# Kernel optimization log

Hardware: AMD Instinct MI355X
Metric: run time of the kernel (lower is better)

## Reference

```python
import jax, jax.numpy as jnp
import numpy as np

S, E, K, D = 50000, 20000, 128, 128  # students, exercises, knowledge, emb dim
NE = 800000                          # edges per polarity
B = 8192                             # batch of response logs
L = 3                                # gcn layers
TEMP, CONTROL = 0.2, 0.3


def setup_inputs() -> dict:
    key = jax.random.key(0)
    ks = jax.random.split(key, 40)

    def nrm(i, shape, scale=0.05):
        return jax.random.normal(ks[i], shape, jnp.float32) * scale

    def uni(i, shape):
        return jax.random.uniform(ks[i], shape, jnp.float32)

    inp = {
        'stu_id': jax.random.randint(ks[0], (B,), 0, S, jnp.int32),
        'exer_id': jax.random.randint(ks[1], (B,), 0, E, jnp.int32),
        'kn_emb': uni(2, (B, K)),
        'ui1_u': jax.random.randint(ks[3], (NE,), 0, S, jnp.int32),
        'ui1_i': jax.random.randint(ks[4], (NE,), 0, E, jnp.int32),
        'ui1_val': uni(5, (NE,)), 'iu1_val': uni(6, (NE,)),
        'eps_ui1': uni(7, (NE,)), 'eps_iu1': uni(8, (NE,)),
        'ui0_u': jax.random.randint(ks[9], (NE,), 0, S, jnp.int32),
        'ui0_i': jax.random.randint(ks[10], (NE,), 0, E, jnp.int32),
        'ui0_val': uni(11, (NE,)), 'iu0_val': uni(12, (NE,)),
        'eps_ui0': uni(13, (NE,)), 'eps_iu0': uni(14, (NE,)),
        # embeddings
        'student_emb': nrm(15, (S, D)), 'exercise_emb': nrm(16, (E, D)),
        'knowledge_emb': nrm(17, (K, D)),
        'stu_b': nrm(18, (S, 1)), 'exer_b': nrm(19, (E, 1)), 'disc': nrm(20, (E, 1)),
        # edge-gate MLPs (polarity 1 and 0)
        'W1_l1': nrm(21, (D, 2 * D)), 'b1_l1': jnp.zeros((D,), jnp.float32),
        'W2_l1': nrm(22, (1, D)), 'b2_l1': jnp.zeros((1,), jnp.float32),
        'W1_l0': nrm(23, (D, 2 * D)), 'b1_l0': jnp.zeros((D,), jnp.float32),
        'W2_l0': nrm(24, (1, D)), 'b2_l0': jnp.zeros((1,), jnp.float32),
        # PosLinear prednet
        'pw1': nrm(25, (256, K)), 'pb1': jnp.zeros((256,), jnp.float32),
        'pw2': nrm(26, (128, 256)), 'pb2': jnp.zeros((128,), jnp.float32),
        'pw3': nrm(27, (1, 128)), 'pb3': jnp.zeros((1,), jnp.float32),
    }
    return inp


def _gate(uids, iids, uemb, iemb, W1, b1, W2, b2, eps):
    # concrete-distribution edge gate; embeddings are detached in original code
    row = jax.lax.stop_gradient(uemb)[uids]          # [NE, D]
    col = jax.lax.stop_gradient(iemb)[iids]          # [NE, D]
    h = jax.nn.relu(jnp.concatenate([row, col], axis=1) @ W1.T + b1)
    logit = (h @ W2.T + b2).reshape(-1)              # [NE]
    eps = jnp.clip(eps, 1e-6, 1.0 - 1e-6)
    g = jnp.log(eps) - jnp.log1p(-eps)               # logistic noise
    return CONTROL * jax.nn.sigmoid((logit + g) / TEMP) + (1.0 - CONTROL)


def _spmm(rows, cols, vals, x, n_rows):
    # out[rows] += vals * x[cols]
    return jax.ops.segment_sum(vals[:, None] * x[cols], rows, num_segments=n_rows)


def _poslin(x, W, b):
    Wp = 2.0 * jax.nn.relu(-W) + W  # == |W|
    return x @ Wp.T + b


def reference(stu_id, exer_id, kn_emb, ui1_u, ui1_i, ui1_val, iu1_val, eps_ui1,
              eps_iu1, ui0_u, ui0_i, ui0_val, iu0_val, eps_ui0, eps_iu0,
              student_emb, exercise_emb, knowledge_emb, stu_b, exer_b, disc,
              W1_l1, b1_l1, W2_l1, b2_l1, W1_l0, b1_l0, W2_l0, b2_l0,
              pw1, pb1, pw2, pb2, pw3, pb3):
    # --- graph_learner: per-edge gates on all 4 sparse matrices ---
    v_ui1 = ui1_val * _gate(ui1_u, ui1_i, student_emb, exercise_emb, W1_l1, b1_l1, W2_l1, b2_l1, eps_ui1)
    v_iu1 = iu1_val * _gate(ui1_u, ui1_i, student_emb, exercise_emb, W1_l1, b1_l1, W2_l1, b2_l1, eps_iu1)
    v_ui0 = ui0_val * _gate(ui0_u, ui0_i, student_emb, exercise_emb, W1_l0, b1_l0, W2_l0, b2_l0, eps_ui0)
    v_iu0 = iu0_val * _gate(ui0_u, ui0_i, student_emb, exercise_emb, W1_l0, b1_l0, W2_l0, b2_l0, eps_iu0)

    # --- graph_representations: L rounds of sparse propagation, mean over layers ---
    stu, exer = student_emb, exercise_emb
    stu_sum, exer_sum = stu, exer
    for _ in range(L):
        u1 = _spmm(ui1_u, ui1_i, v_ui1, exer, S)
        i1 = _spmm(ui1_i, ui1_u, v_iu1, stu, E)
        u0 = _spmm(ui0_u, ui0_i, v_ui0, exer, S)
        i0 = _spmm(ui0_i, ui0_u, v_iu0, stu, E)
        stu, exer = u1 + u0, i1 + i0
        stu_sum = stu_sum + stu
        exer_sum = exer_sum + exer
    stu_final = stu_sum / (L + 1)
    exer_final = exer_sum / (L + 1)

    # --- NCDM-style prediction head with PosLinear MLP ---
    stat = jax.nn.sigmoid(stu_final[stu_id] @ knowledge_emb.T + stu_b[stu_id])   # [B, K]
    diff = jax.nn.sigmoid(exer_final[exer_id] @ knowledge_emb.T + exer_b[exer_id])
    e_d = jax.nn.sigmoid(disc[exer_id])                                          # [B, 1]
    x = e_d * (stat - diff) * kn_emb
    h = jax.nn.sigmoid(_poslin(x, pw1, pb1))
    h = jax.nn.sigmoid(_poslin(h, pw2, pb2))
    out = jax.nn.sigmoid(_poslin(h, pw3, pb3)).reshape(-1)                       # [B]
    return out
```

## Files before the change

### kernel.cpp

```cpp
#include <hip/hip_runtime.h>
#include <hip/hip_bf16.h>
#include <math.h>

#define S_N 50000
#define E_N 20000
#define K_N 128
#define D_N 128
#define NE_N 800000
#define B_N 8192
#define L_N 3
#define GATE_TILES (NE_N / 64)
#define NB_S 782
#define NB_E 313
#define BPAD 464
#define BSLACK 480

typedef __attribute__((ext_vector_type(4))) float floatx4;
typedef __attribute__((ext_vector_type(8))) short short8v;

__device__ __forceinline__ unsigned short f2bf(float x) {
  unsigned int u = __float_as_uint(x);
  u += 0x7FFFu + ((u >> 16) & 1u);
  return (unsigned short)(u >> 16);
}
__device__ __forceinline__ float bf2f(unsigned short u) {
  return __uint_as_float(((unsigned int)u) << 16);
}
__device__ __forceinline__ float sigm(float z) { return 1.0f / (1.0f + __expf(-z)); }

__device__ __forceinline__ unsigned char f2e4m3(float x) {
  unsigned int u = __float_as_uint(x);
  unsigned char s = (unsigned char)((u >> 24) & 0x80);
  int e = (int)((u >> 23) & 0xFF) - 127;
  unsigned int m = u & 0x7FFFFF;
  if (((u >> 23) & 0xFF) == 0) return s;
  if (e >= 9) return s | 0x7E;
  if (e < -10) return s;
  if (e >= -6) {
    unsigned int keep = m >> 20;
    unsigned int rest = m & 0xFFFFF;
    if (rest > 0x80000u || (rest == 0x80000u && (keep & 1))) keep++;
    if (keep == 8) { keep = 0; e++; if (e >= 9) return s | 0x7E; }
    unsigned char b = (unsigned char)(s | ((e + 7) << 3) | keep);
    if ((b & 0x7F) == 0x7F) b = s | 0x7E;
    return b;
  }
  int shift = -6 - e;
  unsigned int full = 0x800000u | m;
  unsigned int q = full >> (20 + shift);
  unsigned int rest = full & ((1u << (20 + shift)) - 1);
  unsigned int half = 1u << (19 + shift);
  if (rest > half || (rest == half && (q & 1))) q++;
  if (q == 8) return s | 0x08;
  return (unsigned char)(s | q);
}
__device__ __forceinline__ unsigned int pk4_fp8(float4 v) {
  return (unsigned int)f2e4m3(v.x) | ((unsigned int)f2e4m3(v.y) << 8) |
         ((unsigned int)f2e4m3(v.z) << 16) | ((unsigned int)f2e4m3(v.w) << 24);
}

__global__ void prep_kernel(const float* __restrict__ W1_l1, const float* __restrict__ W1_l0,
                            const float* __restrict__ pw1, const float* __restrict__ pw2,
                            const float* __restrict__ pw3, const float* __restrict__ ke,
                            unsigned int* __restrict__ w1f8_1, unsigned int* __restrict__ w1f8_0,
                            float* __restrict__ pw1T, float* __restrict__ pw2T,
                            float* __restrict__ pw3a, float* __restrict__ keT) {
  int i = blockIdx.x * blockDim.x + threadIdx.x;
  if (i < 8192) { w1f8_1[i] = pk4_fp8(((const float4*)W1_l1)[i]); return; }
  i -= 8192;
  if (i < 8192) { w1f8_0[i] = pk4_fp8(((const float4*)W1_l0)[i]); return; }
  i -= 8192;
  if (i < 32768) { int d = i >> 8, j = i & 255; pw1T[i] = fabsf(pw1[j * 128 + d]); return; }
  i -= 32768;
  if (i < 32768) { int d = i >> 7, j = i & 127; pw2T[i] = fabsf(pw2[j * 256 + d]); return; }
  i -= 32768;
  if (i < 128) { pw3a[i] = fabsf(pw3[i]); return; }
  i -= 128;
  if (i < 16384) { int d = i >> 7, k = i & 127; keT[i] = ke[k * 128 + d]; return; }
}

__global__ void init_bf_kernel(const float* __restrict__ se, const float* __restrict__ ee,
                               unsigned short* __restrict__ sbf, unsigned short* __restrict__ ebf,
                               unsigned int* __restrict__ sf8, unsigned int* __restrict__ ef8,
                               float* __restrict__ sS, float* __restrict__ eS) {
  int i = blockIdx.x * blockDim.x + threadIdx.x;
  const int nS4 = S_N * 32, nE4 = E_N * 32;
  if (i < nS4) {
    float4 v = ((const float4*)se)[i];
    ((float4*)sS)[i] = v;
    unsigned int lo = (unsigned int)f2bf(v.x) | ((unsigned int)f2bf(v.y) << 16);
    unsigned int hi = (unsigned int)f2bf(v.z) | ((unsigned int)f2bf(v.w) << 16);
    ((uint2*)sbf)[i] = make_uint2(lo, hi);
    sf8[i] = pk4_fp8(v);
    return;
  }
  i -= nS4;
  if (i < nE4) {
    float4 v = ((const float4*)ee)[i];
    ((float4*)eS)[i] = v;
    unsigned int lo = (unsigned int)f2bf(v.x) | ((unsigned int)f2bf(v.y) << 16);
    unsigned int hi = (unsigned int)f2bf(v.z) | ((unsigned int)f2bf(v.w) << 16);
    ((uint2*)ebf)[i] = make_uint2(lo, hi);
    ef8[i] = pk4_fp8(v);
  }
}

__global__ void zero_kernel(int* __restrict__ p, int n) {
  int i = blockIdx.x * blockDim.x + threadIdx.x;
  if (i < n) p[i] = 0;
}

__global__ __launch_bounds__(256)
void histB_kernel(const int* __restrict__ u1, const int* __restrict__ i1,
                  const int* __restrict__ u0, const int* __restrict__ i0,
                  int* __restrict__ gHistS, int* __restrict__ gHistE) {
  __shared__ int hS[NB_S], hE[NB_E];
  int t = threadIdx.x;
  for (int b = t; b < NB_S; b += 256) hS[b] = 0;
  for (int b = t; b < NB_E; b += 256) hE[b] = 0;
  __syncthreads();
  int e0 = blockIdx.x * 2048;
  for (int k = 0; k < 8; ++k) {
    int e = e0 + k * 256 + t;
    if (e < NE_N) {
      atomicAdd(&hS[u1[e] >> 6], 1);
      atomicAdd(&hS[u0[e] >> 6], 1);
      atomicAdd(&hE[i1[e] >> 6], 1);
      atomicAdd(&hE[i0[e] >> 6], 1);
    }
  }
  __syncthreads();
  for (int b = t; b < NB_S; b += 256) if (hS[b]) atomicAdd(&gHistS[b], hS[b]);
  for (int b = t; b < NB_E; b += 256) if (hE[b]) atomicAdd(&gHistE[b], hE[b]);
}

__global__ __launch_bounds__(128)
void scanB_kernel(const int* __restrict__ gHistS, int* __restrict__ baseS,
                  int* __restrict__ gCurS, int* __restrict__ basePS,
                  const int* __restrict__ gHistE, int* __restrict__ baseE,
                  int* __restrict__ gCurE, int* __restrict__ basePE) {
  int w = threadIdx.x >> 6, l = threadIdx.x & 63;
  int n = w ? NB_E : NB_S;
  const int* src = w ? gHistE : gHistS;
  int* bs  = w ? baseE  : baseS;
  int* cur = w ? gCurE  : gCurS;
  int* bsP = w ? basePE : basePS;
  int carry = 0, carryP = 0;
  for (int base = 0; base < n; base += 64) {
    int i = base + l;
    int v = (i < n) ? src[i] : 0;
    int p = (i < n) ? ((v + BPAD + 15) & ~15) : 0;
    int x = v, y = p;
#pragma unroll
    for (int o = 1; o < 64; o <<= 1) {
      int xx = __shfl_up(x, o, 64);
      int yy = __shfl_up(y, o, 64);
      if (l >= o) { x += xx; y += yy; }
    }
    if (i < n) {
      int ex = carry + x - v;
      bs[i] = ex; cur[i] = ex;
      bsP[i] = carryP + y - p;
    }
    carry += __shfl(x, 63, 64);
    carryP += __shfl(y, 63, 64);
  }
  if (l == 0) { bs[n] = carry; bsP[n] = carryP; }
}

__global__ __launch_bounds__(256)
void append_kernel(const int* __restrict__ u1, const int* __restrict__ i1,
                   const int* __restrict__ u0, const int* __restrict__ i0,
                   const float* __restrict__ v_ui1, const float* __restrict__ v_iu1,
                   const float* __restrict__ v_ui0, const float* __restrict__ v_iu0,
                   int* __restrict__ gCurS, int* __restrict__ gCurE,
                   int2* __restrict__ recS, int2* __restrict__ recE) {
  __shared__ int hS[NB_S], hE[NB_E];
  int t = threadIdx.x;
  for (int b = t; b < NB_S; b += 256) hS[b] = 0;
  for (int b = t; b < NB_E; b += 256) hE[b] = 0;
  __syncthreads();
  int e0 = blockIdx.x * 2048;
  for (int k = 0; k < 8; ++k) {
    int e = e0 + k * 256 + t;
    if (e < NE_N) {
      atomicAdd(&hS[u1[e] >> 6], 1);
      atomicAdd(&hS[u0[e] >> 6], 1);
      atomicAdd(&hE[i1[e] >> 6], 1);
      atomicAdd(&hE[i0[e] >> 6], 1);
    }
  }
  __syncthreads();
  for (int b = t; b < NB_S; b += 256) { int c = hS[b]; hS[b] = c ? atomicAdd(&gCurS[b], c) : 0; }
  for (int b = t; b < NB_E; b += 256) { int c = hE[b]; hE[b] = c ? atomicAdd(&gCurE[b], c) : 0; }
  __syncthreads();
  for (int k = 0; k < 8; ++k) {
    int e = e0 + k * 256 + t;
    if (e < NE_N) {
      int a = u1[e], b = i1[e], c = u0[e], d = i0[e];
      int s;
      s = atomicAdd(&hS[a >> 6], 1); recS[s] = make_int2(((a & 63) << 16) | b, __float_as_int(v_ui1[e]));
      s = atomicAdd(&hE[b >> 6], 1); recE[s] = make_int2(((b & 63) << 16) | a, __float_as_int(v_iu1[e]));
      s = atomicAdd(&hS[c >> 6], 1); recS[s] = make_int2(((c & 63) << 16) | d, __float_as_int(v_ui0[e]));
      s = atomicAdd(&hE[d >> 6], 1); recE[s] = make_int2(((d & 63) << 16) | c, __float_as_int(v_iu0[e]));
    }
  }
}

__global__ __launch_bounds__(256)
void sortRow_kernel(const int* __restrict__ baseIn, const int* __restrict__ basePad,
                    const int2* __restrict__ rin_all, int2* __restrict__ rout_all,
                    int* __restrict__ rowPtr, int* __restrict__ rowCnt8, int nRowsTot) {
  __shared__ int cntR[64], offR[64], curR[64];
  int b = blockIdx.x, t = threadIdx.x;
  int bi = baseIn[b], cnt = baseIn[b + 1] - bi;
  int bo = basePad[b];
  int row0 = b * 64;
  const int2* rin = rin_all + bi;
  int2* rout = rout_all + bo;
  if (t < 64) cntR[t] = 0;
  __syncthreads();
  for (int j = t; j < cnt; j += 256) atomicAdd(&cntR[(rin[j].x >> 16) & 63], 1);
  __syncthreads();
  if (t < 64) {
    int p = (cntR[t] + 7) & ~7;
    int x = p;
#pragma unroll
    for (int o = 1; o < 64; o <<= 1) { int y = __shfl_up(x, o, 64); if (t >= o) x += y; }
    int ex = x - p;
    offR[t] = ex; curR[t] = ex;
    if (row0 + t < nRowsTot) {
      rowPtr[row0 + t] = bo + ex;
      rowCnt8[row0 + t] = p >> 3;
    }
  }
  __syncthreads();
  for (int j = t; j < cnt; j += 256) {
    int2 rc = rin[j];
    int r = (rc.x >> 16) & 63;
    int slot = atomicAdd(&curR[r], 1);
    rout[slot] = make_int2(rc.x & 0xFFFF, rc.y);
  }
  __syncthreads();
  if (t < 64) {
    int c = cntR[t], p = (c + 7) & ~7, o = offR[t];
    for (int j = c; j < p; ++j) rout[o + j] = make_int2(0, 0);
  }
}

__global__ __launch_bounds__(512, 2)
void gate_kernel(const int* __restrict__ eu1, const int* __restrict__ ei1,
                 const int* __restrict__ eu0, const int* __restrict__ ei0,
                 const unsigned char* __restrict__ sf8, const unsigned char* __restrict__ ef8,
                 const unsigned char* __restrict__ w1f8_1, const unsigned char* __restrict__ w1f8_0,
                 const float* __restrict__ b1_1, const float* __restrict__ w2_1,
                 const float* __restrict__ b2_1,
                 const float* __restrict__ b1_0, const float* __restrict__ w2_0,
                 const float* __restrict__ b2_0,
                 float* __restrict__ logit1, float* __restrict__ logit0) {
  __shared__ unsigned char Xl[64 * 272];
  __shared__ float plds[8][16];
  const int* eu; const int* ei; const unsigned char* w1f8;
  const float *b1p, *w2p, *b2p; float* lg;
  if (blockIdx.x < 2048) {
    eu = eu1; ei = ei1; w1f8 = w1f8_1; b1p = b1_1; w2p = w2_1; b2p = b2_1; lg = logit1;
  } else {
    eu = eu0; ei = ei0; w1f8 = w1f8_0; b1p = b1_0; w2p = w2_0; b2p = b2_0; lg = logit0;
  }
  int bb = blockIdx.x & 2047;
  int t = threadIdx.x;
  int wv = t >> 6, l = t & 63;
  int sub = l & 15, grp = l >> 4;
  int nh = wv & 1, rg = wv >> 1;

  long bfrag[4][8];
#pragma unroll
  for (int nt = 0; nt < 4; ++nt) {
    int col = nh * 64 + nt * 16 + sub;
#pragma unroll
    for (int ks = 0; ks < 8; ++ks)
      bfrag[nt][ks] = *(const long*)&w1f8[(col << 8) + ks * 32 + grp * 8];
  }
  float b1v[4], w2v[4];
#pragma unroll
  for (int nt = 0; nt < 4; ++nt) {
    int col = nh * 64 + nt * 16 + sub;
    b1v[nt] = b1p[col];
    w2v[nt] = w2p[col];
  }
  float b2s = b2p[0];

  for (int tile = bb; tile < GATE_TILES; tile += 2048) {
    int e0 = tile * 64;
    {
      int el = t >> 3, q = t & 7;
      int eIdx = e0 + el;
      const unsigned char* srcrow = (q < 4)
          ? sf8 + (size_t)eu[eIdx] * 128 + q * 32
          : ef8 + (size_t)ei[eIdx] * 128 + (q - 4) * 32;
      uint4 c0 = ((const uint4*)srcrow)[0];
      uint4 c1 = ((const uint4*)srcrow)[1];
      *(uint4*)&Xl[el * 272 + q * 32] = c0;
      *(uint4*)&Xl[el * 272 + q * 32 + 16] = c1;
    }
    __syncthreads();

    floatx4 zero4 = {0.f, 0.f, 0.f, 0.f};
    floatx4 acc[4] = {zero4, zero4, zero4, zero4};
#pragma unroll
    for (int ks = 0; ks < 8; ++ks) {
      long a = *(const long*)&Xl[(rg * 16 + sub) * 272 + ks * 32 + grp * 8];
#pragma unroll
      for (int nt = 0; nt < 4; ++nt)
        acc[nt] = __builtin_amdgcn_mfma_f32_16x16x32_fp8_fp8(a, bfrag[nt][ks], acc[nt], 0, 0, 0);
    }
    float p0 = 0, p1 = 0, p2 = 0, p3 = 0;
#pragma unroll
    for (int nt = 0; nt < 4; ++nt) {
      float bb2 = b1v[nt], ww = w2v[nt];
      p0 += fmaxf(acc[nt][0] + bb2, 0.0f) * ww;
      p1 += fmaxf(acc[nt][1] + bb2, 0.0f) * ww;
      p2 += fmaxf(acc[nt][2] + bb2, 0.0f) * ww;
      p3 += fmaxf(acc[nt][3] + bb2, 0.0f) * ww;
    }
#pragma unroll
    for (int m = 1; m < 16; m <<= 1) {
      p0 += __shfl_xor(p0, m, 64);
      p1 += __shfl_xor(p1, m, 64);
      p2 += __shfl_xor(p2, m, 64);
      p3 += __shfl_xor(p3, m, 64);
    }
    if (sub < 4) {
      float pv = (sub == 0) ? p0 : (sub == 1) ? p1 : (sub == 2) ? p2 : p3;
      plds[wv][grp * 4 + sub] = pv;
    }
    __syncthreads();
    if (wv == 0)
      lg[e0 + l] = plds[(l >> 4) * 2][l & 15] + plds[(l >> 4) * 2 + 1][l & 15] + b2s;
    __syncthreads();
  }
}

__global__ __launch_bounds__(256)
void gatefin_kernel(const float* __restrict__ logit1, const float* __restrict__ logit0,
                    const float* __restrict__ ui1_val, const float* __restrict__ iu1_val,
                    const float* __restrict__ eps_ui1, const float* __restrict__ eps_iu1,
                    const float* __restrict__ ui0_val, const float* __restrict__ iu0_val,
                    const float* __restrict__ eps_ui0, const float* __restrict__ eps_iu0,
                    float* __restrict__ v_ui1, float* __restrict__ v_iu1,
                    float* __restrict__ v_ui0, float* __restrict__ v_iu0) {
  int e = blockIdx.x * 256 + threadIdx.x;
  if (e >= NE_N) return;
  float lg1 = logit1[e], lg0 = logit0[e];
  float ep, g, s;
  ep = fminf(fmaxf(eps_ui1[e], 1e-6f), 1.0f - 1e-6f);
  g = __logf(ep) - log1pf(-ep);
  s = 1.0f / (1.0f + __expf(-(lg1 + g) * 5.0f));
  v_ui1[e] = ui1_val[e] * (0.3f * s + 0.7f);
  ep = fminf(fmaxf(eps_iu1[e], 1e-6f), 1.0f - 1e-6f);
  g = __logf(ep) - log1pf(-ep);
  s = 1.0f / (1.0f + __expf(-(lg1 + g) * 5.0f));
  v_iu1[e] = iu1_val[e] * (0.3f * s + 0.7f);
  ep = fminf(fmaxf(eps_ui0[e], 1e-6f), 1.0f - 1e-6f);
  g = __logf(ep) - log1pf(-ep);
  s = 1.0f / (1.0f + __expf(-(lg0 + g) * 5.0f));
  v_ui0[e] = ui0_val[e] * (0.3f * s + 0.7f);
  ep = fminf(fmaxf(eps_iu0[e], 1e-6f), 1.0f - 1e-6f);
  g = __logf(ep) - log1pf(-ep);
  s = 1.0f / (1.0f + __expf(-(lg0 + g) * 5.0f));
  v_iu0[e] = iu0_val[e] * (0.3f * s + 0.7f);
}

__global__ __launch_bounds__(256)
void spmm_csr_kernel(const int* __restrict__ rowPtrS, const int* __restrict__ rowCnt8S,
                     const int2* __restrict__ rec2S,
                     const int* __restrict__ rowPtrE, const int* __restrict__ rowCnt8E,
                     const int2* __restrict__ rec2E,
                     const unsigned short* __restrict__ scur, const unsigned short* __restrict__ ecur,
                     unsigned short* __restrict__ snxt, unsigned short* __restrict__ enxt,
                     float* __restrict__ stuS, float* __restrict__ exeS) {
  int gw = (blockIdx.x * 256 + threadIdx.x) >> 6;
  int l = threadIdx.x & 63;
  int g = l >> 3, lane8 = l & 7;
  if (gw >= S_N + E_N) return;
  const int2* rec; const unsigned short* src; unsigned short* dst; float* sum;
  const int* rp; const int* rc8; int r;
  if (gw < S_N) { r = gw;       rp = rowPtrS; rc8 = rowCnt8S; rec = rec2S; src = ecur; dst = snxt; sum = stuS; }
  else          { r = gw - S_N; rp = rowPtrE; rc8 = rowCnt8E; rec = rec2E; src = scur; dst = enxt; sum = exeS; }
  int s0 = rp[r], n8 = rc8[r];
  float acc[16];
#pragma unroll
  for (int i = 0; i < 16; ++i) acc[i] = 0.f;
  for (int k = 0; k < n8; ++k) {
    int2 e = rec[s0 + k * 8 + g];
    float val = __int_as_float(e.y);
    const uint4* rowp = (const uint4*)(src + (size_t)e.x * 128);
    uint4 q0 = rowp[lane8 * 2];
    uint4 q1 = rowp[lane8 * 2 + 1];
#pragma unroll
    for (int i = 0; i < 4; ++i) {
      unsigned int w = ((const unsigned int*)&q0)[i];
      acc[2 * i]     = fmaf(val, bf2f((unsigned short)(w & 0xFFFF)), acc[2 * i]);
      acc[2 * i + 1] = fmaf(val, bf2f((unsigned short)(w >> 16)),    acc[2 * i + 1]);
    }
#pragma unroll
    for (int i = 0; i < 4; ++i) {
      unsigned int w = ((const unsigned int*)&q1)[i];
      acc[8 + 2 * i]     = fmaf(val, bf2f((unsigned short)(w & 0xFFFF)), acc[8 + 2 * i]);
      acc[8 + 2 * i + 1] = fmaf(val, bf2f((unsigned short)(w >> 16)),    acc[8 + 2 * i + 1]);
    }
  }
#pragma unroll
  for (int m = 8; m < 64; m <<= 1) {
#pragma unroll
    for (int i = 0; i < 16; ++i) acc[i] += __shfl_xor(acc[i], m, 64);
  }
  if (g == 0) {
    size_t base = (size_t)r * 128 + lane8 * 16;
    short8v o0, o1;
#pragma unroll
    for (int i = 0; i < 8; ++i) { o0[i] = (short)f2bf(acc[i]); o1[i] = (short)f2bf(acc[8 + i]); }
    *(short8v*)(dst + base) = o0;
    *(short8v*)(dst + base + 8) = o1;
    float4* sp = (float4*)(sum + base);
#pragma unroll
    for (int i = 0; i < 4; ++i) {
      float4 s = sp[i];
      s.x += acc[4 * i]; s.y += acc[4 * i + 1]; s.z += acc[4 * i + 2]; s.w += acc[4 * i + 3];
      sp[i] = s;
    }
  }
}

__global__ __launch_bounds__(256)
void head1_kernel(const int* __restrict__ stu_id, const int* __restrict__ exer_id,
                  const float* __restrict__ kn, const float* __restrict__ stuS,
                  const float* __restrict__ exeS, const float* __restrict__ keT,
                  const float* __restrict__ stub, const float* __restrict__ exeb,
                  const float* __restrict__ disc, float* __restrict__ xbuf) {
  __shared__ float srw[4][128], erw[4][128];
  int wv = threadIdx.x >> 6, l = threadIdx.x & 63;
  int b = blockIdx.x * 4 + wv;
  int sid = stu_id[b], eid = exer_id[b];
  float2 sv = ((const float2*)(stuS + (size_t)sid * 128))[l];
  float2 ev = ((const float2*)(exeS + (size_t)eid * 128))[l];
  srw[wv][2 * l] = sv.x * 0.25f; srw[wv][2 * l + 1] = sv.y * 0.25f;
  erw[wv][2 * l] = ev.x * 0.25f; erw[wv][2 * l + 1] = ev.y * 0.25f;
  __syncthreads();
  float s0 = 0, s1 = 0, d0 = 0, d1 = 0;
  for (int d = 0; d < 128; ++d) {
    float sd = srw[wv][d], ed = erw[wv][d];
    float ka = keT[d * 128 + l], kb = keT[d * 128 + l + 64];
    s0 = fmaf(sd, ka, s0); s1 = fmaf(sd, kb, s1);
    d0 = fmaf(ed, ka, d0); d1 = fmaf(ed, kb, d1);
  }
  float sbv = stub[sid], ebv = exeb[eid];
  float edv = sigm(disc[eid]);
  float st0 = sigm(s0 + sbv), st1 = sigm(s1 + sbv);
  float df0 = sigm(d0 + ebv), df1 = sigm(d1 + ebv);
  xbuf[(size_t)b * 128 + l]      = edv * (st0 - df0) * kn[(size_t)b * 128 + l];
  xbuf[(size_t)b * 128 + l + 64] = edv * (st1 - df1) * kn[(size_t)b * 128 + l + 64];
}

__global__ __launch_bounds__(256)
void head2_kernel(const float* __restrict__ xbuf, const float* __restrict__ pw1T,
                  const float* __restrict__ pb1, const float* __restrict__ pw2T,
                  const float* __restrict__ pb2, const float* __restrict__ pw3a,
                  const float* __restrict__ pb3, float* __restrict__ out) {
  __shared__ float xs[4][128], h1s[4][256], h2s[4][128];
  int wv = threadIdx.x >> 6, l = threadIdx.x & 63;
  int b = blockIdx.x * 4 + wv;
  xs[wv][l] = xbuf[(size_t)b * 128 + l];
  xs[wv][l + 64] = xbuf[(size_t)b * 128 + l + 64];
  __syncthreads();
#pragma unroll
  for (int q = 0; q < 4; ++q) {
    int j = q * 64 + l;
    float acc = 0.f;
    for (int d = 0; d < 128; ++d) acc = fmaf(xs[wv][d], pw1T[d * 256 + j], acc);
    h1s[wv][j] = sigm(acc + pb1[j]);
  }
  __syncthreads();
#pragma unroll
  for (int q = 0; q < 2; ++q) {
    int j = q * 64 + l;
    float acc = 0.f;
    for (int d = 0; d < 256; ++d) acc = fmaf(h1s[wv][d], pw2T[d * 128 + j], acc);
    h2s[wv][j] = sigm(acc + pb2[j]);
  }
  __syncthreads();
  float p = h2s[wv][l] * pw3a[l] + h2s[wv][l + 64] * pw3a[l + 64];
#pragma unroll
  for (int m = 1; m < 64; m <<= 1) p += __shfl_xor(p, m, 64);
  if (l == 0) out[b] = sigm(p + pb3[0]);
}

extern "C" void kernel_launch(void* const* d_in, const int* in_sizes, int n_in,
                              void* d_out, int out_size, void* d_ws, size_t ws_size,
                              hipStream_t stream) {
  const int*   stu_id  = (const int*)  d_in[0];
  const int*   exer_id = (const int*)  d_in[1];
  const float* kn_emb  = (const float*)d_in[2];
  const int*   ui1_u   = (const int*)  d_in[3];
  const int*   ui1_i   = (const int*)  d_in[4];
  const float* ui1_val = (const float*)d_in[5];
  const float* iu1_val = (const float*)d_in[6];
  const float* eps_ui1 = (const float*)d_in[7];
  const float* eps_iu1 = (const float*)d_in[8];
  const int*   ui0_u   = (const int*)  d_in[9];
  const int*   ui0_i   = (const int*)  d_in[10];
  const float* ui0_val = (const float*)d_in[11];
  const float* iu0_val = (const float*)d_in[12];
  const float* eps_ui0 = (const float*)d_in[13];
  const float* eps_iu0 = (const float*)d_in[14];
  const float* stu_emb = (const float*)d_in[15];
  const float* exe_emb = (const float*)d_in[16];
  const float* kno_emb = (const float*)d_in[17];
  const float* stu_b   = (const float*)d_in[18];
  const float* exe_b   = (const float*)d_in[19];
  const float* disc    = (const float*)d_in[20];
  const float* W1_l1   = (const float*)d_in[21];
  const float* b1_l1   = (const float*)d_in[22];
  const float* W2_l1   = (const float*)d_in[23];
  const float* b2_l1   = (const float*)d_in[24];
  const float* W1_l0   = (const float*)d_in[25];
  const float* b1_l0   = (const float*)d_in[26];
  const float* W2_l0   = (const float*)d_in[27];
  const float* b2_l0   = (const float*)d_in[28];
  const float* pw1     = (const float*)d_in[29];
  const float* pb1     = (const float*)d_in[30];
  const float* pw2     = (const float*)d_in[31];
  const float* pb2     = (const float*)d_in[32];
  const float* pw3     = (const float*)d_in[33];
  const float* pb3     = (const float*)d_in[34];
  float* out = (float*)d_out;
  (void)in_sizes; (void)n_in; (void)out_size; (void)ws_size;

  size_t off = 0;
  char* base = (char*)d_ws;
  auto carve = [&](size_t bytes) -> char* {
    char* p = base + off;
    off += (bytes + 255) & ~(size_t)255;
    return p;
  };
  unsigned int* w1f8_1 = (unsigned int*)carve(8192 * 4);
  unsigned int* w1f8_0 = (unsigned int*)carve(8192 * 4);
  float* pw1T = (float*)carve(32768 * 4);
  float* pw2T = (float*)carve(32768 * 4);
  float* pw3a = (float*)carve(128 * 4);
  float* keT  = (float*)carve(16384 * 4);
  float* v_ui1 = (float*)carve((size_t)2 * NE_N * 8 + (size_t)BSLACK * NB_S * 8);
  float* v_iu1 = v_ui1 + NE_N;
  float* v_ui0 = v_iu1 + NE_N;
  float* v_iu0 = v_ui0 + NE_N;
  unsigned short* stuBfA = (unsigned short*)carve((size_t)S_N * 128 * 2);
  unsigned short* stuBfB = (unsigned short*)carve((size_t)S_N * 128 * 2);
  unsigned short* exeBfA = (unsigned short*)carve((size_t)E_N * 128 * 2);
  unsigned short* exeBfB = (unsigned short*)carve((size_t)E_N * 128 * 2);
  unsigned int* sf8 = (unsigned int*)carve((size_t)S_N * 32 * 4);
  unsigned int* ef8 = (unsigned int*)carve((size_t)E_N * 32 * 4);
  float* stuS = (float*)carve((size_t)S_N * 128 * 4);
  float* exeS = (float*)carve((size_t)E_N * 128 * 4);
  float* logit1 = (float*)carve((size_t)NE_N * 4);
  float* logit0 = (float*)carve((size_t)NE_N * 4);
  int* gHistS = (int*)carve((size_t)(NB_S + NB_E) * 4);
  int* gHistE = gHistS + NB_S;
  int* baseSb  = (int*)carve((size_t)(NB_S + 1) * 4);
  int* baseEb  = (int*)carve((size_t)(NB_E + 1) * 4);
  int* basePSb = (int*)carve((size_t)(NB_S + 1) * 4);
  int* basePEb = (int*)carve((size_t)(NB_E + 1) * 4);
  int* gCurS  = (int*)carve((size_t)NB_S * 4);
  int* gCurE  = (int*)carve((size_t)NB_E * 4);
  int2* recS = (int2*)carve((size_t)2 * NE_N * 8 + (size_t)BSLACK * NB_E * 8);
  int2* recE = (int2*)carve((size_t)2 * NE_N * 8);
  int* rowPtrS  = (int*)carve((size_t)S_N * 4);
  int* rowCnt8S = (int*)carve((size_t)S_N * 4);
  int* rowPtrE  = (int*)carve((size_t)E_N * 4);
  int* rowCnt8E = (int*)carve((size_t)E_N * 4);
  float* xbuf = (float*)carve((size_t)B_N * 128 * 4);
  int2* rec2S = (int2*)v_ui1;
  int2* rec2E = recS;

  prep_kernel<<<(98432 + 255) / 256, 256, 0, stream>>>(W1_l1, W1_l0, pw1, pw2, pw3, kno_emb,
                                                       w1f8_1, w1f8_0, pw1T, pw2T, pw3a, keT);
  init_bf_kernel<<<(2240000 + 255) / 256, 256, 0, stream>>>(stu_emb, exe_emb, stuBfA, exeBfA,
                                                            sf8, ef8, stuS, exeS);
  zero_kernel<<<(NB_S + NB_E + 255) / 256, 256, 0, stream>>>(gHistS, NB_S + NB_E);
  histB_kernel<<<(NE_N + 2047) / 2048, 256, 0, stream>>>(ui1_u, ui1_i, ui0_u, ui0_i,
                                                         gHistS, gHistE);
  scanB_kernel<<<1, 128, 0, stream>>>(gHistS, baseSb, gCurS, basePSb,
                                      gHistE, baseEb, gCurE, basePEb);
  gate_kernel<<<4096, 512, 0, stream>>>(ui1_u, ui1_i, ui0_u, ui0_i,
                                        (const unsigned char*)sf8, (const unsigned char*)ef8,
                                        (const unsigned char*)w1f8_1, (const unsigned char*)w1f8_0,
                                        b1_l1, W2_l1, b2_l1, b1_l0, W2_l0, b2_l0,
                                        logit1, logit0);
  gatefin_kernel<<<(NE_N + 255) / 256, 256, 0, stream>>>(logit1, logit0,
                                                         ui1_val, iu1_val, eps_ui1, eps_iu1,
                                                         ui0_val, iu0_val, eps_ui0, eps_iu0,
                                                         v_ui1, v_iu1, v_ui0, v_iu0);
  append_kernel<<<(NE_N + 2047) / 2048, 256, 0, stream>>>(ui1_u, ui1_i, ui0_u, ui0_i,
                                                          v_ui1, v_iu1, v_ui0, v_iu0,
                                                          gCurS, gCurE, recS, recE);
  sortRow_kernel<<<NB_S, 256, 0, stream>>>(baseSb, basePSb, recS, rec2S,
                                           rowPtrS, rowCnt8S, S_N);
  sortRow_kernel<<<NB_E, 256, 0, stream>>>(baseEb, basePEb, recE, rec2E,
                                           rowPtrE, rowCnt8E, E_N);
  const unsigned short* scur = stuBfA; const unsigned short* ecur = exeBfA;
  unsigned short* snxt = stuBfB; unsigned short* enxt = exeBfB;
  for (int layer = 0; layer < L_N; ++layer) {
    spmm_csr_kernel<<<(S_N + E_N + 3) / 4, 256, 0, stream>>>(
        rowPtrS, rowCnt8S, rec2S, rowPtrE, rowCnt8E, rec2E,
        scur, ecur, snxt, enxt, stuS, exeS);
    const unsigned short* t1 = scur; scur = snxt; snxt = (unsigned short*)t1;
    const unsigned short* t2 = ecur; ecur = enxt; enxt = (unsigned short*)t2;
  }
  head1_kernel<<<B_N / 4, 256, 0, stream>>>(stu_id, exer_id, kn_emb, stuS, exeS, keT,
                                            stu_b, exe_b, disc, xbuf);
  head2_kernel<<<B_N / 4, 256, 0, stream>>>(xbuf, pw1T, pb1, pw2T, pb2, pw3a, pb3, out);
}
```

Baseline: 704.8 us.

## Bucket-sort edges by student before gate MLP for gather locality

Adds a permute pass that bucket-sorts each polarity's edges by student block (64-student buckets), so the gate kernel gathers student fp8 rows with better cache locality. It also swizzles the LDS layout of the gathered tile to reduce bank conflicts. Gate blocks now process contiguous chunks of tiles. gatefin and append consume the permuted order, using stored original edge indices for val/eps lookups. This adds an extra histogram-and-scatter pass and indirect reads in gatefin.

Result: slower. 794.2 us (+12.7%).

```diff
diff --git a/kernel.cpp b/kernel.cpp
--- a/kernel.cpp
+++ b/kernel.cpp
@@ -113,43 +113,53 @@
 __global__ __launch_bounds__(256)
 void histB_kernel(const int* __restrict__ u1, const int* __restrict__ i1,
                   const int* __restrict__ u0, const int* __restrict__ i0,
-                  int* __restrict__ gHistS, int* __restrict__ gHistE) {
-  __shared__ int hS[NB_S], hE[NB_E];
+                  int* __restrict__ gHistS, int* __restrict__ gHistE,
+                  int* __restrict__ gH1, int* __restrict__ gH0) {
+  __shared__ int hS[NB_S], hE[NB_E], h1[NB_S], h0[NB_S];
   int t = threadIdx.x;
-  for (int b = t; b < NB_S; b += 256) hS[b] = 0;
+  for (int b = t; b < NB_S; b += 256) { hS[b] = 0; h1[b] = 0; h0[b] = 0; }
   for (int b = t; b < NB_E; b += 256) hE[b] = 0;
   __syncthreads();
   int e0 = blockIdx.x * 2048;
   for (int k = 0; k < 8; ++k) {
     int e = e0 + k * 256 + t;
     if (e < NE_N) {
-      atomicAdd(&hS[u1[e] >> 6], 1);
-      atomicAdd(&hS[u0[e] >> 6], 1);
+      int a = u1[e] >> 6, c = u0[e] >> 6;
+      atomicAdd(&hS[a], 1);
+      atomicAdd(&hS[c], 1);
       atomicAdd(&hE[i1[e] >> 6], 1);
       atomicAdd(&hE[i0[e] >> 6], 1);
-    }
-  }
-  __syncthreads();
-  for (int b = t; b < NB_S; b += 256) if (hS[b]) atomicAdd(&gHistS[b], hS[b]);
+      atomicAdd(&h1[a], 1);
+      atomicAdd(&h0[c], 1);
+    }
+  }
+  __syncthreads();
+  for (int b = t; b < NB_S; b += 256) {
+    if (hS[b]) atomicAdd(&gHistS[b], hS[b]);
+    if (h1[b]) atomicAdd(&gH1[b], h1[b]);
+    if (h0[b]) atomicAdd(&gH0[b], h0[b]);
+  }
   for (int b = t; b < NB_E; b += 256) if (hE[b]) atomicAdd(&gHistE[b], hE[b]);
 }
 
-__global__ __launch_bounds__(128)
-void scanB_kernel(const int* __restrict__ gHistS, int* __restrict__ baseS,
-                  int* __restrict__ gCurS, int* __restrict__ basePS,
+__global__ __launch_bounds__(256)
+void scan4_kernel(const int* __restrict__ gHistS, int* __restrict__ baseS,
+                  int* __restrict__ curS, int* __restrict__ basePS,
                   const int* __restrict__ gHistE, int* __restrict__ baseE,
-                  int* __restrict__ gCurE, int* __restrict__ basePE) {
+                  int* __restrict__ curE, int* __restrict__ basePE,
+                  const int* __restrict__ gH1, int* __restrict__ base1, int* __restrict__ cur1,
+                  const int* __restrict__ gH0, int* __restrict__ base0, int* __restrict__ cur0) {
   int w = threadIdx.x >> 6, l = threadIdx.x & 63;
-  int n = w ? NB_E : NB_S;
-  const int* src = w ? gHistE : gHistS;
-  int* bs  = w ? baseE  : baseS;
-  int* cur = w ? gCurE  : gCurS;
-  int* bsP = w ? basePE : basePS;
+  const int* src; int n; int* bs; int* cur; int* bsP;
+  if (w == 0)      { src = gHistS; n = NB_S; bs = baseS; cur = curS; bsP = basePS; }
+  else if (w == 1) { src = gHistE; n = NB_E; bs = baseE; cur = curE; bsP = basePE; }
+  else if (w == 2) { src = gH1;    n = NB_S; bs = base1; cur = cur1; bsP = nullptr; }
+  else             { src = gH0;    n = NB_S; bs = base0; cur = cur0; bsP = nullptr; }
   int carry = 0, carryP = 0;
   for (int base = 0; base < n; base += 64) {
     int i = base + l;
     int v = (i < n) ? src[i] : 0;
-    int p = (i < n) ? ((v + BPAD + 15) & ~15) : 0;
+    int p = (i < n && bsP) ? ((v + BPAD + 15) & ~15) : 0;
     int x = v, y = p;
 #pragma unroll
     for (int o = 1; o < 64; o <<= 1) {
@@ -160,19 +170,182 @@
     if (i < n) {
       int ex = carry + x - v;
       bs[i] = ex; cur[i] = ex;
-      bsP[i] = carryP + y - p;
+      if (bsP) bsP[i] = carryP + y - p;
     }
     carry += __shfl(x, 63, 64);
     carryP += __shfl(y, 63, 64);
   }
-  if (l == 0) { bs[n] = carry; bsP[n] = carryP; }
-}
-
-__global__ __launch_bounds__(256)
-void append_kernel(const int* __restrict__ u1, const int* __restrict__ i1,
-                   const int* __restrict__ u0, const int* __restrict__ i0,
-                   const float* __restrict__ v_ui1, const float* __restrict__ v_iu1,
-                   const float* __restrict__ v_ui0, const float* __restrict__ v_iu0,
+  if (l == 0) { bs[n] = carry; if (bsP) bsP[n] = carryP; }
+}
+
+__global__ __launch_bounds__(256)
+void permute_kernel(const int* __restrict__ u1, const int* __restrict__ i1,
+                    const int* __restrict__ u0, const int* __restrict__ i0,
+                    int* __restrict__ cur1, int* __restrict__ cur0,
+                    int2* __restrict__ upi1, int* __restrict__ op1,
+                    int2* __restrict__ upi0, int* __restrict__ op0) {
+  __shared__ int h1[NB_S], h0[NB_S];
+  int t = threadIdx.x;
+  for (int b = t; b < NB_S; b += 256) { h1[b] = 0; h0[b] = 0; }
+  __syncthreads();
+  int e0 = blockIdx.x * 2048;
+  for (int k = 0; k < 8; ++k) {
+    int e = e0 + k * 256 + t;
+    if (e < NE_N) {
+      atomicAdd(&h1[u1[e] >> 6], 1);
+      atomicAdd(&h0[u0[e] >> 6], 1);
+    }
+  }
+  __syncthreads();
+  for (int b = t; b < NB_S; b += 256) { int c = h1[b]; h1[b] = c ? atomicAdd(&cur1[b], c) : 0; }
+  for (int b = t; b < NB_S; b += 256) { int c = h0[b]; h0[b] = c ? atomicAdd(&cur0[b], c) : 0; }
+  __syncthreads();
+  for (int k = 0; k < 8; ++k) {
+    int e = e0 + k * 256 + t;
+    if (e < NE_N) {
+      int a = u1[e], c = u0[e];
+      int j = atomicAdd(&h1[a >> 6], 1);
+      upi1[j] = make_int2(a, i1[e]); op1[j] = e;
+      j = atomicAdd(&h0[c >> 6], 1);
+      upi0[j] = make_int2(c, i0[e]); op0[j] = e;
+    }
+  }
+}
+
+__global__ __launch_bounds__(512, 2)
+void gate_kernel(const int2* __restrict__ upi1, const int2* __restrict__ upi0,
+                 const unsigned char* __restrict__ sf8, const unsigned char* __restrict__ ef8,
+                 const unsigned char* __restrict__ w1f8_1, const unsigned char* __restrict__ w1f8_0,
+                 const float* __restrict__ b1_1, const float* __restrict__ w2_1,
+                 const float* __restrict__ b2_1,
+                 const float* __restrict__ b1_0, const float* __restrict__ w2_0,
+                 const float* __restrict__ b2_0,
+                 float* __restrict__ lgP1, float* __restrict__ lgP0) {
+  __shared__ unsigned char Xl[64 * 272];
+  __shared__ float plds[8][16];
+  const int2* upi; const unsigned char* w1f8;
+  const float *b1p, *w2p, *b2p; float* lg;
+  if (blockIdx.x < 2048) {
+    upi = upi1; w1f8 = w1f8_1; b1p = b1_1; w2p = w2_1; b2p = b2_1; lg = lgP1;
+  } else {
+    upi = upi0; w1f8 = w1f8_0; b1p = b1_0; w2p = w2_0; b2p = b2_0; lg = lgP0;
+  }
+  int bb = blockIdx.x & 2047;
+  int chunk = (bb & 7) * 256 + (bb >> 3);
+  int tBeg = chunk * 7;
+  int tEnd = tBeg + 7; if (tEnd > GATE_TILES) tEnd = GATE_TILES;
+  if (tBeg >= GATE_TILES) return;
+  int t = threadIdx.x;
+  int wv = t >> 6, l = t & 63;
+  int sub = l & 15, grp = l >> 4;
+  int nh = wv & 1, rg = wv >> 1;
+
+  long bfrag[4][8];
+#pragma unroll
+  for (int nt = 0; nt < 4; ++nt) {
+    int col = nh * 64 + nt * 16 + sub;
+#pragma unroll
+    for (int ks = 0; ks < 8; ++ks)
+      bfrag[nt][ks] = *(const long*)&w1f8[(col << 8) + ks * 32 + grp * 8];
+  }
+  float b1v[4], w2v[4];
+#pragma unroll
+  for (int nt = 0; nt < 4; ++nt) {
+    int col = nh * 64 + nt * 16 + sub;
+    b1v[nt] = b1p[col];
+    w2v[nt] = w2p[col];
+  }
+  float b2s = b2p[0];
+
+  for (int tile = tBeg; tile < tEnd; ++tile) {
+    int e0 = tile * 64;
+    {
+      int el = t >> 3, q = t & 7;
+      int2 ui = upi[e0 + el];
+      const unsigned char* srcrow = (q < 4)
+          ? sf8 + (size_t)ui.x * 128 + q * 32
+          : ef8 + (size_t)ui.y * 128 + (q - 4) * 32;
+      int qs = q ^ (el & 7);
+      uint4 c0 = ((const uint4*)srcrow)[0];
+      uint4 c1 = ((const uint4*)srcrow)[1];
+      *(uint4*)&Xl[el * 272 + qs * 32] = c0;
+      *(uint4*)&Xl[el * 272 + qs * 32 + 16] = c1;
+    }
+    __syncthreads();
+
+    floatx4 zero4 = {0.f, 0.f, 0.f, 0.f};
+    floatx4 acc[4] = {zero4, zero4, zero4, zero4};
+#pragma unroll
+    for (int ks = 0; ks < 8; ++ks) {
+      int row = rg * 16 + sub;
+      long a = *(const long*)&Xl[row * 272 + ((ks ^ (sub & 7)) << 5) + grp * 8];
+#pragma unroll
+      for (int nt = 0; nt < 4; ++nt)
+        acc[nt] = __builtin_amdgcn_mfma_f32_16x16x32_fp8_fp8(a, bfrag[nt][ks], acc[nt], 0, 0, 0);
+    }
+    float p0 = 0, p1 = 0, p2 = 0, p3 = 0;
+#pragma unroll
+    for (int nt = 0; nt < 4; ++nt) {
+      float bb2 = b1v[nt], ww = w2v[nt];
+      p0 += fmaxf(acc[nt][0] + bb2, 0.0f) * ww;
+      p1 += fmaxf(acc[nt][1] + bb2, 0.0f) * ww;
+      p2 += fmaxf(acc[nt][2] + bb2, 0.0f) * ww;
+      p3 += fmaxf(acc[nt][3] + bb2, 0.0f) * ww;
+    }
+#pragma unroll
+    for (int m = 1; m < 16; m <<= 1) {
+      p0 += __shfl_xor(p0, m, 64);
+      p1 += __shfl_xor(p1, m, 64);
+      p2 += __shfl_xor(p2, m, 64);
+      p3 += __shfl_xor(p3, m, 64);
+    }
+    if (sub < 4) {
+      float pv = (sub == 0) ? p0 : (sub == 1) ? p1 : (sub == 2) ? p2 : p3;
+      plds[wv][grp * 4 + sub] = pv;
+    }
+    __syncthreads();
+    if (wv == 0)
+      lg[e0 + l] = plds[(l >> 4) * 2][l & 15] + plds[(l >> 4) * 2 + 1][l & 15] + b2s;
+    __syncthreads();
+  }
+}
+
+__global__ __launch_bounds__(256)
+void gatefin_kernel(const float* __restrict__ lgP1, const float* __restrict__ lgP0,
+                    const int* __restrict__ op1, const int* __restrict__ op0,
+                    const float* __restrict__ ui1_val, const float* __restrict__ iu1_val,
+                    const float* __restrict__ eps_ui1, const float* __restrict__ eps_iu1,
+                    const float* __restrict__ ui0_val, const float* __restrict__ iu0_val,
+                    const float* __restrict__ eps_ui0, const float* __restrict__ eps_iu0,
+                    float* __restrict__ vP1ui, float* __restrict__ vP1iu,
+                    float* __restrict__ vP0ui, float* __restrict__ vP0iu) {
+  int j = blockIdx.x * 256 + threadIdx.x;
+  if (j >= NE_N) return;
+  float lg1 = lgP1[j], lg0 = lgP0[j];
+  int e1 = op1[j], e0 = op0[j];
+  float ep, g, s;
+  ep = fminf(fmaxf(eps_ui1[e1], 1e-6f), 1.0f - 1e-6f);
+  g = __logf(ep) - log1pf(-ep);
+  s = 1.0f / (1.0f + __expf(-(lg1 + g) * 5.0f));
+  vP1ui[j] = ui1_val[e1] * (0.3f * s + 0.7f);
+  ep = fminf(fmaxf(eps_iu1[e1], 1e-6f), 1.0f - 1e-6f);
+  g = __logf(ep) - log1pf(-ep);
+  s = 1.0f / (1.0f + __expf(-(lg1 + g) * 5.0f));
+  vP1iu[j] = iu1_val[e1] * (0.3f * s + 0.7f);
+  ep = fminf(fmaxf(eps_ui0[e0], 1e-6f), 1.0f - 1e-6f);
+  g = __logf(ep) - log1pf(-ep);
+  s = 1.0f / (1.0f + __expf(-(lg0 + g) * 5.0f));
+  vP0ui[j] = ui0_val[e0] * (0.3f * s + 0.7f);
+  ep = fminf(fmaxf(eps_iu0[e0], 1e-6f), 1.0f - 1e-6f);
+  g = __logf(ep) - log1pf(-ep);
+  s = 1.0f / (1.0f + __expf(-(lg0 + g) * 5.0f));
+  vP0iu[j] = iu0_val[e0] * (0.3f * s + 0.7f);
+}
+
+__global__ __launch_bounds__(256)
+void append_kernel(const int2* __restrict__ upi1, const int2* __restrict__ upi0,
+                   const float* __restrict__ vP1ui, const float* __restrict__ vP1iu,
+                   const float* __restrict__ vP0ui, const float* __restrict__ vP0iu,
                    int* __restrict__ gCurS, int* __restrict__ gCurE,
                    int2* __restrict__ recS, int2* __restrict__ recE) {
   __shared__ int hS[NB_S], hE[NB_E];
@@ -182,12 +355,13 @@
   __syncthreads();
   int e0 = blockIdx.x * 2048;
   for (int k = 0; k < 8; ++k) {
-    int e = e0 + k * 256 + t;
-    if (e < NE_N) {
-      atomicAdd(&hS[u1[e] >> 6], 1);
-      atomicAdd(&hS[u0[e] >> 6], 1);
-      atomicAdd(&hE[i1[e] >> 6], 1);
-      atomicAdd(&hE[i0[e] >> 6], 1);
+    int j = e0 + k * 256 + t;
+    if (j < NE_N) {
+      int2 p1 = upi1[j]; int2 p0 = upi0[j];
+      atomicAdd(&hS[p1.x >> 6], 1);
+      atomicAdd(&hS[p0.x >> 6], 1);
+      atomicAdd(&hE[p1.y >> 6], 1);
+      atomicAdd(&hE[p0.y >> 6], 1);
     }
   }
   __syncthreads();
@@ -195,14 +369,15 @@
   for (int b = t; b < NB_E; b += 256) { int c = hE[b]; hE[b] = c ? atomicAdd(&gCurE[b], c) : 0; }
   __syncthreads();
   for (int k = 0; k < 8; ++k) {
-    int e = e0 + k * 256 + t;
-    if (e < NE_N) {
-      int a = u1[e], b = i1[e], c = u0[e], d = i0[e];
+    int j = e0 + k * 256 + t;
+    if (j < NE_N) {
+      int2 p1 = upi1[j]; int2 p0 = upi0[j];
+      int a = p1.x, b = p1.y, c = p0.x, d = p0.y;
       int s;
-      s = atomicAdd(&hS[a >> 6], 1); recS[s] = make_int2(((a & 63) << 16) | b, __float_as_int(v_ui1[e]));
-      s = atomicAdd(&hE[b >> 6], 1); recE[s] = make_int2(((b & 63) << 16) | a, __float_as_int(v_iu1[e]));
-      s = atomicAdd(&hS[c >> 6], 1); recS[s] = make_int2(((c & 63) << 16) | d, __float_as_int(v_ui0[e]));
-      s = atomicAdd(&hE[d >> 6], 1); recE[s] = make_int2(((d & 63) << 16) | c, __float_as_int(v_iu0[e]));
+      s = atomicAdd(&hS[a >> 6], 1); recS[s] = make_int2(((a & 63) << 16) | b, __float_as_int(vP1ui[j]));
+      s = atomicAdd(&hE[b >> 6], 1); recE[s] = make_int2(((b & 63) << 16) | a, __float_as_int(vP1iu[j]));
+      s = atomicAdd(&hS[c >> 6], 1); recS[s] = make_int2(((c & 63) << 16) | d, __float_as_int(vP0ui[j]));
+      s = atomicAdd(&hE[d >> 6], 1); recE[s] = make_int2(((d & 63) << 16) | c, __float_as_int(vP0iu[j]));
     }
   }
 }
@@ -246,129 +421,6 @@
     int c = cntR[t], p = (c + 7) & ~7, o = offR[t];
     for (int j = c; j < p; ++j) rout[o + j] = make_int2(0, 0);
   }
-}
-
-__global__ __launch_bounds__(512, 2)
-void gate_kernel(const int* __restrict__ eu1, const int* __restrict__ ei1,
-                 const int* __restrict__ eu0, const int* __restrict__ ei0,
-                 const unsigned char* __restrict__ sf8, const unsigned char* __restrict__ ef8,
-                 const unsigned char* __restrict__ w1f8_1, const unsigned char* __restrict__ w1f8_0,
-                 const float* __restrict__ b1_1, const float* __restrict__ w2_1,
-                 const float* __restrict__ b2_1,
-                 const float* __restrict__ b1_0, const float* __restrict__ w2_0,
-                 const float* __restrict__ b2_0,
-                 float* __restrict__ logit1, float* __restrict__ logit0) {
-  __shared__ unsigned char Xl[64 * 272];
-  __shared__ float plds[8][16];
-  const int* eu; const int* ei; const unsigned char* w1f8;
-  const float *b1p, *w2p, *b2p; float* lg;
-  if (blockIdx.x < 2048) {
-    eu = eu1; ei = ei1; w1f8 = w1f8_1; b1p = b1_1; w2p = w2_1; b2p = b2_1; lg = logit1;
-  } else {
-    eu = eu0; ei = ei0; w1f8 = w1f8_0; b1p = b1_0; w2p = w2_0; b2p = b2_0; lg = logit0;
-  }
-  int bb = blockIdx.x & 2047;
-  int t = threadIdx.x;
-  int wv = t >> 6, l = t & 63;
-  int sub = l & 15, grp = l >> 4;
-  int nh = wv & 1, rg = wv >> 1;
-
-  long bfrag[4][8];
-#pragma unroll
-  for (int nt = 0; nt < 4; ++nt) {
-    int col = nh * 64 + nt * 16 + sub;
-#pragma unroll
-    for (int ks = 0; ks < 8; ++ks)
-      bfrag[nt][ks] = *(const long*)&w1f8[(col << 8) + ks * 32 + grp * 8];
-  }
-  float b1v[4], w2v[4];
-#pragma unroll
-  for (int nt = 0; nt < 4; ++nt) {
-    int col = nh * 64 + nt * 16 + sub;
-    b1v[nt] = b1p[col];
-    w2v[nt] = w2p[col];
-  }
-  float b2s = b2p[0];
-
-  for (int tile = bb; tile < GATE_TILES; tile += 2048) {
-    int e0 = tile * 64;
-    {
-      int el = t >> 3, q = t & 7;
-      int eIdx = e0 + el;
-      const unsigned char* srcrow = (q < 4)
-          ? sf8 + (size_t)eu[eIdx] * 128 + q * 32
-          : ef8 + (size_t)ei[eIdx] * 128 + (q - 4) * 32;
-      uint4 c0 = ((const uint4*)srcrow)[0];
-      uint4 c1 = ((const uint4*)srcrow)[1];
-      *(uint4*)&Xl[el * 272 + q * 32] = c0;
-      *(uint4*)&Xl[el * 272 + q * 32 + 16] = c1;
-    }
-    __syncthreads();
-
-    floatx4 zero4 = {0.f, 0.f, 0.f, 0.f};
-    floatx4 acc[4] = {zero4, zero4, zero4, zero4};
-#pragma unroll
-    for (int ks = 0; ks < 8; ++ks) {
-      long a = *(const long*)&Xl[(rg * 16 + sub) * 272 + ks * 32 + grp * 8];
-#pragma unroll
-      for (int nt = 0; nt < 4; ++nt)
-        acc[nt] = __builtin_amdgcn_mfma_f32_16x16x32_fp8_fp8(a, bfrag[nt][ks], acc[nt], 0, 0, 0);
-    }
-    float p0 = 0, p1 = 0, p2 = 0, p3 = 0;
-#pragma unroll
-    for (int nt = 0; nt < 4; ++nt) {
-      float bb2 = b1v[nt], ww = w2v[nt];
-      p0 += fmaxf(acc[nt][0] + bb2, 0.0f) * ww;
-      p1 += fmaxf(acc[nt][1] + bb2, 0.0f) * ww;
-      p2 += fmaxf(acc[nt][2] + bb2, 0.0f) * ww;
-      p3 += fmaxf(acc[nt][3] + bb2, 0.0f) * ww;
-    }
-#pragma unroll
-    for (int m = 1; m < 16; m <<= 1) {
-      p0 += __shfl_xor(p0, m, 64);
-      p1 += __shfl_xor(p1, m, 64);
-      p2 += __shfl_xor(p2, m, 64);
-      p3 += __shfl_xor(p3, m, 64);
-    }
-    if (sub < 4) {
-      float pv = (sub == 0) ? p0 : (sub == 1) ? p1 : (sub == 2) ? p2 : p3;
-      plds[wv][grp * 4 + sub] = pv;
-    }
-    __syncthreads();
-    if (wv == 0)
-      lg[e0 + l] = plds[(l >> 4) * 2][l & 15] + plds[(l >> 4) * 2 + 1][l & 15] + b2s;
-    __syncthreads();
-  }
-}
-
-__global__ __launch_bounds__(256)
-void gatefin_kernel(const float* __restrict__ logit1, const float* __restrict__ logit0,
-                    const float* __restrict__ ui1_val, const float* __restrict__ iu1_val,
-                    const float* __restrict__ eps_ui1, const float* __restrict__ eps_iu1,
-                    const float* __restrict__ ui0_val, const float* __restrict__ iu0_val,
-                    const float* __restrict__ eps_ui0, const float* __restrict__ eps_iu0,
-                    float* __restrict__ v_ui1, float* __restrict__ v_iu1,
-                    float* __restrict__ v_ui0, float* __restrict__ v_iu0) {
-  int e = blockIdx.x * 256 + threadIdx.x;
-  if (e >= NE_N) return;
-  float lg1 = logit1[e], lg0 = logit0[e];
-  float ep, g, s;
-  ep = fminf(fmaxf(eps_ui1[e], 1e-6f), 1.0f - 1e-6f);
-  g = __logf(ep) - log1pf(-ep);
-  s = 1.0f / (1.0f + __expf(-(lg1 + g) * 5.0f));
-  v_ui1[e] = ui1_val[e] * (0.3f * s + 0.7f);
-  ep = fminf(fmaxf(eps_iu1[e], 1e-6f), 1.0f - 1e-6f);
-  g = __logf(ep) - log1pf(-ep);
-  s = 1.0f / (1.0f + __expf(-(lg1 + g) * 5.0f));
-  v_iu1[e] = iu1_val[e] * (0.3f * s + 0.7f);
-  ep = fminf(fmaxf(eps_ui0[e], 1e-6f), 1.0f - 1e-6f);
-  g = __logf(ep) - log1pf(-ep);
-  s = 1.0f / (1.0f + __expf(-(lg0 + g) * 5.0f));
-  v_ui0[e] = ui0_val[e] * (0.3f * s + 0.7f);
-  ep = fminf(fmaxf(eps_iu0[e], 1e-6f), 1.0f - 1e-6f);
-  g = __logf(ep) - log1pf(-ep);
-  s = 1.0f / (1.0f + __expf(-(lg0 + g) * 5.0f));
-  v_iu0[e] = iu0_val[e] * (0.3f * s + 0.7f);
 }
 
 __global__ __launch_bounds__(256)
@@ -549,28 +601,37 @@
   float* pw2T = (float*)carve(32768 * 4);
   float* pw3a = (float*)carve(128 * 4);
   float* keT  = (float*)carve(16384 * 4);
-  float* v_ui1 = (float*)carve((size_t)2 * NE_N * 8 + (size_t)BSLACK * NB_S * 8);
-  float* v_iu1 = v_ui1 + NE_N;
-  float* v_ui0 = v_iu1 + NE_N;
-  float* v_iu0 = v_ui0 + NE_N;
+  char* vblock = carve((size_t)2 * NE_N * 8 + (size_t)BSLACK * NB_S * 8);
+  int2* upi1 = (int2*)vblock;
+  int2* upi0 = (int2*)vblock + NE_N;
   unsigned short* stuBfA = (unsigned short*)carve((size_t)S_N * 128 * 2);
   unsigned short* stuBfB = (unsigned short*)carve((size_t)S_N * 128 * 2);
+  int*   op1   = (int*)stuBfB;
+  int*   op0   = (int*)stuBfB + NE_N;
+  float* vP1iu = (float*)((int*)stuBfB + 2 * NE_N);
+  float* vP0iu = (float*)((int*)stuBfB + 3 * NE_N);
   unsigned short* exeBfA = (unsigned short*)carve((size_t)E_N * 128 * 2);
   unsigned short* exeBfB = (unsigned short*)carve((size_t)E_N * 128 * 2);
   unsigned int* sf8 = (unsigned int*)carve((size_t)S_N * 32 * 4);
   unsigned int* ef8 = (unsigned int*)carve((size_t)E_N * 32 * 4);
   float* stuS = (float*)carve((size_t)S_N * 128 * 4);
   float* exeS = (float*)carve((size_t)E_N * 128 * 4);
-  float* logit1 = (float*)carve((size_t)NE_N * 4);
-  float* logit0 = (float*)carve((size_t)NE_N * 4);
-  int* gHistS = (int*)carve((size_t)(NB_S + NB_E) * 4);
+  float* lgP1 = (float*)carve((size_t)NE_N * 4);
+  float* lgP0 = (float*)carve((size_t)NE_N * 4);
+  int* gHistS = (int*)carve((size_t)(NB_S + NB_E + 2 * NB_S) * 4);
   int* gHistE = gHistS + NB_S;
+  int* gH1 = gHistE + NB_E;
+  int* gH0 = gH1 + NB_S;
   int* baseSb  = (int*)carve((size_t)(NB_S + 1) * 4);
   int* baseEb  = (int*)carve((size_t)(NB_E + 1) * 4);
   int* basePSb = (int*)carve((size_t)(NB_S + 1) * 4);
   int* basePEb = (int*)carve((size_t)(NB_E + 1) * 4);
   int* gCurS  = (int*)carve((size_t)NB_S * 4);
   int* gCurE  = (int*)carve((size_t)NB_E * 4);
+  int* base1  = (int*)carve((size_t)(NB_S + 1) * 4);
+  int* cur1   = (int*)carve((size_t)NB_S * 4);
+  int* base0  = (int*)carve((size_t)(NB_S + 1) * 4);
+  int* cur0   = (int*)carve((size_t)NB_S * 4);
   int2* recS = (int2*)carve((size_t)2 * NE_N * 8 + (size_t)BSLACK * NB_E * 8);
   int2* recE = (int2*)carve((size_t)2 * NE_N * 8);
   int* rowPtrS  = (int*)carve((size_t)S_N * 4);
@@ -578,29 +639,35 @@
   int* rowPtrE  = (int*)carve((size_t)E_N * 4);
   int* rowCnt8E = (int*)carve((size_t)E_N * 4);
   float* xbuf = (float*)carve((size_t)B_N * 128 * 4);
-  int2* rec2S = (int2*)v_ui1;
+  int2* rec2S = (int2*)vblock;
   int2* rec2E = recS;
+  float* vP1ui = lgP1;
+  float* vP0ui = lgP0;
 
   prep_kernel<<<(98432 + 255) / 256, 256, 0, stream>>>(W1_l1, W1_l0, pw1, pw2, pw3, kno_emb,
                                                        w1f8_1, w1f8_0, pw1T, pw2T, pw3a, keT);
   init_bf_kernel<<<(2240000 + 255) / 256, 256, 0, stream>>>(stu_emb, exe_emb, stuBfA, exeBfA,
                                                             sf8, ef8, stuS, exeS);
-  zero_kernel<<<(NB_S + NB_E + 255) / 256, 256, 0, stream>>>(gHistS, NB_S + NB_E);
+  zero_kernel<<<(NB_S + NB_E + 2 * NB_S + 255) / 256, 256, 0, stream>>>(gHistS,
+                                                                        NB_S + NB_E + 2 * NB_S);
   histB_kernel<<<(NE_N + 2047) / 2048, 256, 0, stream>>>(ui1_u, ui1_i, ui0_u, ui0_i,
-                                                         gHistS, gHistE);
-  scanB_kernel<<<1, 128, 0, stream>>>(gHistS, baseSb, gCurS, basePSb,
-                                      gHistE, baseEb, gCurE, basePEb);
-  gate_kernel<<<4096, 512, 0, stream>>>(ui1_u, ui1_i, ui0_u, ui0_i,
+                                                         gHistS, gHistE, gH1, gH0);
+  scan4_kernel<<<1, 256, 0, stream>>>(gHistS, baseSb, gCurS, basePSb,
+                                      gHistE, baseEb, gCurE, basePEb,
+                                      gH1, base1, cur1, gH0, base0, cur0);
+  permute_kernel<<<(NE_N + 2047) / 2048, 256, 0, stream>>>(ui1_u, ui1_i, ui0_u, ui0_i,
+                                                           cur1, cur0, upi1, op1, upi0, op0);
+  gate_kernel<<<4096, 512, 0, stream>>>(upi1, upi0,
                                         (const unsigned char*)sf8, (const unsigned char*)ef8,
                                         (const unsigned char*)w1f8_1, (const unsigned char*)w1f8_0,
                                         b1_l1, W2_l1, b2_l1, b1_l0, W2_l0, b2_l0,
-                                        logit1, logit0);
-  gatefin_kernel<<<(NE_N + 255) / 256, 256, 0, stream>>>(logit1, logit0,
+                                        lgP1, lgP0);
+  gatefin_kernel<<<(NE_N + 255) / 256, 256, 0, stream>>>(lgP1, lgP0, op1, op0,
                                                          ui1_val, iu1_val, eps_ui1, eps_iu1,
                                                          ui0_val, iu0_val, eps_ui0, eps_iu0,
-                                                         v_ui1, v_iu1, v_ui0, v_iu0);
-  append_kernel<<<(NE_N + 2047) / 2048, 256, 0, stream>>>(ui1_u, ui1_i, ui0_u, ui0_i,
-                                                          v_ui1, v_iu1, v_ui0, v_iu0,
+                                                         vP1ui, vP1iu, vP0ui, vP0iu);
+  append_kernel<<<(NE_N + 2047) / 2048, 256, 0, stream>>>(upi1, upi0,
+                                                          vP1ui, vP1iu, vP0ui, vP0iu,
                                                           gCurS, gCurE, recS, recE);
   sortRow_kernel<<<NB_S, 256, 0, stream>>>(baseSb, basePSb, recS, rec2S,
                                            rowPtrS, rowCnt8S, S_N);
```
